# Optimization experiments

Measured on AMD Instinct MI355X. Metric: run time of the kernel, lower is better.

The kernel has to match this reference:

```python
import jax, jax.numpy as jnp
import numpy as np

D = 1024
H = 16
HD = D // H
FFN = D * 2
EPS = 1e-5


def _layernorm(x, g, b):
    mu = jnp.mean(x, axis=-1, keepdims=True)
    var = jnp.var(x, axis=-1, keepdims=True)
    return (x - mu) * jax.lax.rsqrt(var + EPS) * g + b


def setup_inputs() -> dict:
    key = jax.random.key(0)
    ks = jax.random.split(key, 12)
    s = 1.0 / np.sqrt(D)
    inp = {
        "x": jax.random.normal(ks[0], (2, 2048, D), dtype=jnp.float32),
        "Wq": jax.random.normal(ks[1], (D, D), dtype=jnp.float32) * s,
        "bq": jnp.zeros((D,), jnp.float32),
        "Wk": jax.random.normal(ks[2], (D, D), dtype=jnp.float32) * s,
        "bk": jnp.zeros((D,), jnp.float32),
        "Wv": jax.random.normal(ks[3], (D, D), dtype=jnp.float32) * s,
        "bv": jnp.zeros((D,), jnp.float32),
        "Wo": jax.random.normal(ks[4], (D, D), dtype=jnp.float32) * s,
        "bo": jnp.zeros((D,), jnp.float32),
        "g1": jnp.ones((D,), jnp.float32),
        "b1": jnp.zeros((D,), jnp.float32),
        "W_ff1": jax.random.normal(ks[5], (D, FFN), dtype=jnp.float32) * s,
        "b_ff1": jnp.zeros((FFN,), jnp.float32),
        "W_ff2": jax.random.normal(ks[6], (FFN, D), dtype=jnp.float32) * (1.0 / np.sqrt(FFN)),
        "b_ff2": jnp.zeros((D,), jnp.float32),
        "g2": jnp.ones((D,), jnp.float32),
        "b2": jnp.zeros((D,), jnp.float32),
    }
    return inp


def reference(x, Wq, bq, Wk, bk, Wv, bv, Wo, bo, g1, b1, W_ff1, b_ff1, W_ff2, b_ff2, g2, b2):
    B, S, _ = x.shape
    # QKV projections -> [B, H, S, HD]
    def split_heads(t):
        return t.reshape(B, S, H, HD).transpose(0, 2, 1, 3)
    Q = split_heads(x @ Wq + bq)
    K = split_heads(x @ Wk + bk)
    V = split_heads(x @ Wv + bv)
    scores = jnp.einsum('bhqd,bhkd->bhqk', Q, K) / np.sqrt(HD).astype(np.float32)
    attn = jax.nn.softmax(scores, axis=-1)  # dropout = identity in eval
    ctx = jnp.einsum('bhqk,bhkd->bhqd', attn, V)
    ctx = ctx.transpose(0, 2, 1, 3).reshape(B, S, D)
    x = _layernorm(x + ctx @ Wo + bo, g1, b1)
    h = jax.nn.gelu(x @ W_ff1 + b_ff1, approximate=False)
    x = _layernorm(x + h @ W_ff2 + b_ff2, g2, b2)
    return x
```

## Files before the change

kernel.cpp:

```cpp
#include <hip/hip_runtime.h>

#define SEQ 2048
#define NTOK 4096
#define DM 1024
#define LDQK 3072

typedef __attribute__((ext_vector_type(4))) float f32x4;
typedef __attribute__((ext_vector_type(8))) short short8;
typedef __attribute__((ext_vector_type(4))) short short4v;

__device__ __forceinline__ short f2bf(float f) {
  union { float f; unsigned u; } x; x.f = f;
  unsigned r = x.u + 0x7fffu + ((x.u >> 16) & 1u);
  return (short)(r >> 16);
}

__device__ __forceinline__ float bf2f(short s) {
  union { unsigned u; float f; } x;
  x.u = ((unsigned)(unsigned short)s) << 16;
  return x.f;
}

__device__ __forceinline__ void async_load16(const void* g, void* l) {
  __builtin_amdgcn_global_load_lds(
      (const __attribute__((address_space(1))) void*)g,
      (__attribute__((address_space(3))) void*)l, 16, 0, 0);
}

__global__ void __launch_bounds__(256) prep_all(
    const float* __restrict__ Wq, const float* __restrict__ Wk,
    const float* __restrict__ Wv, const float* __restrict__ Wo,
    const float* __restrict__ Wf1, const float* __restrict__ Wf2,
    const float* __restrict__ x,
    short* __restrict__ Wqkv, short* __restrict__ Wto,
    short* __restrict__ Wtf1, short* __restrict__ Wtf2,
    short* __restrict__ xb) {
  const int z = blockIdx.z;
  const int tx = threadIdx.x, ty = threadIdx.y;
  if (z == 6) {
    int blk = blockIdx.y * 64 + blockIdx.x;
    int i = blk * 256 + ty * 32 + tx;
    f32x4 v = ((const f32x4*)x)[i];
    short4v o;
#pragma unroll
    for (int j = 0; j < 4; ++j) o[j] = f2bf(v[j]);
    ((short4v*)xb)[i] = o;
    return;
  }
  const float* in;
  short* out;
  int K, N;
  switch (z) {
    case 0: in = Wq;  out = Wqkv;               K = 1024; N = 1024; break;
    case 1: in = Wk;  out = Wqkv + 1024 * 1024; K = 1024; N = 1024; break;
    case 2: in = Wv;  out = Wqkv + 2048 * 1024; K = 1024; N = 1024; break;
    case 3: in = Wo;  out = Wto;                K = 1024; N = 1024; break;
    case 4: in = Wf1; out = Wtf1;               K = 1024; N = 2048; break;
    default: in = Wf2; out = Wtf2;              K = 2048; N = 1024; break;
  }
  if (blockIdx.x * 32 >= N || blockIdx.y * 32 >= K) return;
  __shared__ float t[32][33];
  const int n = blockIdx.x * 32 + tx;
#pragma unroll
  for (int i = 0; i < 4; ++i) {
    int k = blockIdx.y * 32 + ty + i * 8;
    t[ty + i * 8][tx] = in[(size_t)k * N + n];
  }
  __syncthreads();
  const int k2 = blockIdx.y * 32 + tx;
#pragma unroll
  for (int i = 0; i < 4; ++i) {
    int n2 = blockIdx.x * 32 + ty + i * 8;
    out[(size_t)n2 * K + k2] = f2bf(t[tx][ty + i * 8]);
  }
}

template <int EPI, bool TRIPLE, bool DBUF>
__global__ void __launch_bounds__(256, 2) gemm_bt(
    const short* __restrict__ A, const short* __restrict__ Bt,
    const float* __restrict__ b0, const float* __restrict__ b1,
    const float* __restrict__ b2, void* __restrict__ Cout,
    short* __restrict__ VtOut, int M, int N, int K) {
  __shared__ __align__(16) short As[DBUF ? 2 * 128 * 64 : 128 * 64];
  __shared__ __align__(16) short Bs[DBUF ? 2 * 128 * 64 : 128 * 64];
  const int w = threadIdx.x >> 6, lane = threadIdx.x & 63;
  const int hi = lane >> 4, lo = lane & 15;
  const int bm = blockIdx.y, bn = blockIdx.x;
  const int wr = w >> 1, wc = w & 1;
  f32x4 acc[4][4] = {};
  const int nkt = K >> 6;

  auto stage = [&](int kt, int buf) {
#pragma unroll
    for (int j = 0; j < 4; ++j) {
      int c = (j * 4 + w) * 64 + lane;
      int r = c >> 3;
      int scc = (c & 7) ^ (r & 7);
      async_load16(A + (size_t)(bm * 128 + r) * K + kt * 64 + scc * 8,
                   &As[buf * (128 * 64) + (j * 4 + w) * 512]);
      async_load16(Bt + (size_t)(bn * 128 + r) * K + kt * 64 + scc * 8,
                   &Bs[buf * (128 * 64) + (j * 4 + w) * 512]);
    }
  };

  if (DBUF) {
    stage(0, 0);
    __syncthreads();
  }

  for (int kt = 0; kt < nkt; ++kt) {
    int buf = 0;
    if (DBUF) {
      buf = kt & 1;
      if (kt + 1 < nkt) stage(kt + 1, buf ^ 1);
    } else {
      stage(kt, 0);
      __syncthreads();
    }
#pragma unroll
    for (int ks = 0; ks < 2; ++ks) {
      short8 af[4], bf[4];
#pragma unroll
      for (int m = 0; m < 4; ++m) {
        int row = wr * 64 + m * 16 + lo;
        int ch = (ks * 4 + hi) ^ (row & 7);
        af[m] = *(const short8*)(&As[buf * (128 * 64) + row * 64 + ch * 8]);
      }
#pragma unroll
      for (int n = 0; n < 4; ++n) {
        int row = wc * 64 + n * 16 + lo;
        int ch = (ks * 4 + hi) ^ (row & 7);
        bf[n] = *(const short8*)(&Bs[buf * (128 * 64) + row * 64 + ch * 8]);
      }
#pragma unroll
      for (int m = 0; m < 4; ++m)
#pragma unroll
        for (int n = 0; n < 4; ++n)
          acc[m][n] = __builtin_amdgcn_mfma_f32_16x16x32_bf16(af[m], bf[n], acc[m][n], 0, 0, 0);
    }
    __syncthreads();
  }
  const float* bp = b0;
  if (TRIPLE) { int r = bn >> 3; bp = (r == 0) ? b0 : ((r == 1) ? b1 : b2); }
  const int colb = bn * 128 + wc * 64 + lo;
  if (TRIPLE && bn >= 16) {
#pragma unroll
    for (int m = 0; m < 4; ++m) {
      int row0 = bm * 128 + wr * 64 + m * 16 + hi * 4;
      int bb = row0 >> 11, ss = row0 & 2047;
#pragma unroll
      for (int n = 0; n < 4; ++n) {
        int col = colb + n * 16;
        int vdim = col - 2048;
        int hh = vdim >> 6, dd = vdim & 63;
        float bs = bp[vdim];
        short4v t;
#pragma unroll
        for (int j = 0; j < 4; ++j) t[j] = f2bf(acc[m][n][j] + bs);
        *(short4v*)&VtOut[((size_t)(bb * 16 + hh) * 64 + dd) * SEQ + ss] = t;
      }
    }
    return;
  }
#pragma unroll
  for (int m = 0; m < 4; ++m) {
    int row0 = bm * 128 + wr * 64 + m * 16 + hi * 4;
#pragma unroll
    for (int n = 0; n < 4; ++n) {
      int col = colb + n * 16;
      float bs = bp[TRIPLE ? (col & 1023) : col];
#pragma unroll
      for (int j = 0; j < 4; ++j) {
        float v = acc[m][n][j] + bs;
        if (EPI == 1) v = 0.5f * v * (1.f + erff(v * 0.70710678f));
        ((short*)Cout)[(size_t)(row0 + j) * N + col] = f2bf(v);
      }
    }
  }
}

__global__ void __launch_bounds__(256, 2) gemm_n64(
    const short* __restrict__ A, const short* __restrict__ Bt,
    const float* __restrict__ b0, const short* __restrict__ resid,
    short* __restrict__ Cout, int M, int N, int K) {
  __shared__ __align__(16) short As[2][128 * 64];
  __shared__ __align__(16) short Bs[2][64 * 64];
  const int w = threadIdx.x >> 6, lane = threadIdx.x & 63;
  const int hi = lane >> 4, lo = lane & 15;
  const int bm = blockIdx.y, bn = blockIdx.x;
  const int wr = w >> 1, wc = w & 1;
  f32x4 acc[4][2] = {};
  const int nkt = K >> 6;

  auto stage = [&](int kt, int buf) {
#pragma unroll
    for (int j = 0; j < 4; ++j) {
      int c = (j * 4 + w) * 64 + lane;
      int r = c >> 3;
      int scc = (c & 7) ^ (r & 7);
      async_load16(A + (size_t)(bm * 128 + r) * K + kt * 64 + scc * 8,
                   &As[buf][(j * 4 + w) * 512]);
    }
#pragma unroll
    for (int j = 0; j < 2; ++j) {
      int c = j * 256 + w * 64 + lane;
      int r = c >> 3;
      int scc = (c & 7) ^ (r & 7);
      async_load16(Bt + (size_t)(bn * 64 + r) * K + kt * 64 + scc * 8,
                   &Bs[buf][(j * 256 + w * 64) * 8]);
    }
  };

  stage(0, 0);
  __syncthreads();

  for (int kt = 0; kt < nkt; ++kt) {
    const int buf = kt & 1;
    if (kt + 1 < nkt) stage(kt + 1, buf ^ 1);
#pragma unroll
    for (int ks = 0; ks < 2; ++ks) {
      short8 af[4], bf[2];
#pragma unroll
      for (int m = 0; m < 4; ++m) {
        int row = wr * 64 + m * 16 + lo;
        int ch = (ks * 4 + hi) ^ (row & 7);
        af[m] = *(const short8*)(&As[buf][row * 64 + ch * 8]);
      }
#pragma unroll
      for (int n = 0; n < 2; ++n) {
        int row = wc * 32 + n * 16 + lo;
        int ch = (ks * 4 + hi) ^ (row & 7);
        bf[n] = *(const short8*)(&Bs[buf][row * 64 + ch * 8]);
      }
#pragma unroll
      for (int m = 0; m < 4; ++m)
#pragma unroll
        for (int n = 0; n < 2; ++n)
          acc[m][n] = __builtin_amdgcn_mfma_f32_16x16x32_bf16(af[m], bf[n], acc[m][n], 0, 0, 0);
    }
    __syncthreads();
  }
  const int colb = bn * 64 + wc * 32 + lo;
#pragma unroll
  for (int m = 0; m < 4; ++m) {
    int row0 = bm * 128 + wr * 64 + m * 16 + hi * 4;
#pragma unroll
    for (int n = 0; n < 2; ++n) {
      int col = colb + n * 16;
      float bs = b0[col];
#pragma unroll
      for (int j = 0; j < 4; ++j) {
        size_t idx = (size_t)(row0 + j) * N + col;
        Cout[idx] = f2bf(acc[m][n][j] + bs + bf2f(resid[idx]));
      }
    }
  }
}

__global__ void __launch_bounds__(256, 2) attn_kernel(
    const short* __restrict__ Qb, const short* __restrict__ Kb,
    const short* __restrict__ Vt, short* __restrict__ ctx) {
  const int w = threadIdx.x >> 6, lane = threadIdx.x & 63;
  const int hi = lane >> 4, lo = lane & 15;
  const int tid = threadIdx.x;
  const int L = blockIdx.y * 16 + blockIdx.x;
  const int W = (L & 7) * 64 + (L >> 3);
  const int qt = W & 15, bh = W >> 4;
  const int b = bh >> 4, h = bh & 15;
  const int qbase = qt * 128 + w * 32;
  const float C = 0.18033688f;

  __shared__ __align__(16) short Ks[2][128 * 64];
  __shared__ __align__(16) short Vs[2][64 * 128];
  __shared__ __align__(16) short P[4][16 * 128];

  const short* qp = Qb + (size_t)(b * SEQ + qbase + lo) * LDQK + h * 64;
  short8 bq[2][2];
#pragma unroll
  for (int u = 0; u < 2; ++u)
#pragma unroll
    for (int c = 0; c < 2; ++c)
      bq[u][c] = *(const short8*)(qp + (size_t)u * 16 * LDQK + c * 32 + hi * 8);

  const short* kb = Kb + (size_t)(b * SEQ) * LDQK + h * 64;
  const short* vb = Vt + (size_t)bh * 64 * SEQ;

  auto stage = [&](int kt, int buf) {
    const short* kg = kb + (size_t)(kt * 128) * LDQK;
#pragma unroll
    for (int i = 0; i < 4; ++i) {
      int c = i * 256 + tid;
      int r = c >> 3, scc = (c & 7) ^ (r & 7);
      async_load16(kg + (size_t)r * LDQK + scc * 8,
                   &Ks[buf][(i * 256 + w * 64) * 8]);
    }
    const short* vg = vb + kt * 128;
#pragma unroll
    for (int i = 0; i < 4; ++i) {
      int c = i * 256 + tid;
      int r = c >> 4, sc2 = (c & 15) ^ (r & 7);
      async_load16(vg + (size_t)r * SEQ + sc2 * 8,
                   &Vs[buf][(i * 256 + w * 64) * 8]);
    }
  };

  stage(0, 0);
  __syncthreads();

  f32x4 o[2][4] = {};
  float lacc[2] = {0.f, 0.f};
  const int x7 = lo & 7;

  for (int kt = 0; kt < SEQ / 128; ++kt) {
    const int buf = kt & 1;
    if (kt + 1 < SEQ / 128) stage(kt + 1, buf ^ 1);

    f32x4 s[2][8] = {};
#pragma unroll
    for (int g = 0; g < 8; ++g) {
      const short* kr = &Ks[buf][(g * 16 + lo) * 64];
      short8 ka0 = *(const short8*)(kr + ((hi) ^ x7) * 8);
      short8 ka1 = *(const short8*)(kr + ((4 + hi) ^ x7) * 8);
      s[0][g] = __builtin_amdgcn_mfma_f32_16x16x32_bf16(ka0, bq[0][0], s[0][g], 0, 0, 0);
      s[1][g] = __builtin_amdgcn_mfma_f32_16x16x32_bf16(ka0, bq[1][0], s[1][g], 0, 0, 0);
      s[0][g] = __builtin_amdgcn_mfma_f32_16x16x32_bf16(ka1, bq[0][1], s[0][g], 0, 0, 0);
      s[1][g] = __builtin_amdgcn_mfma_f32_16x16x32_bf16(ka1, bq[1][1], s[1][g], 0, 0, 0);
    }
    short8 vv[4][4];
#pragma unroll
    for (int ks = 0; ks < 4; ++ks)
#pragma unroll
      for (int a = 0; a < 4; ++a)
        vv[ks][a] = *(const short8*)(&Vs[buf][(a * 16 + lo) * 128 + (((ks * 4 + hi) ^ x7) * 8)]);
#pragma unroll
    for (int u = 0; u < 2; ++u) {
      float rsg[8];
      short* pbase = &P[w][0];
#pragma unroll
      for (int g = 0; g < 8; ++g) {
        float p0 = exp2f(s[u][g][0] * C);
        float p1 = exp2f(s[u][g][1] * C);
        float p2 = exp2f(s[u][g][2] * C);
        float p3 = exp2f(s[u][g][3] * C);
        rsg[g] = (p0 + p1) + (p2 + p3);
        unsigned w0, w1;
        asm("v_cvt_pk_bf16_f32 %0, %1, %2" : "=v"(w0) : "v"(p0), "v"(p1));
        asm("v_cvt_pk_bf16_f32 %0, %1, %2" : "=v"(w1) : "v"(p2), "v"(p3));
        union { unsigned uu[2]; short4v s4; } cv;
        cv.uu[0] = w0; cv.uu[1] = w1;
        int pc = (2 * g + (hi >> 1)) ^ x7;
        *(short4v*)(pbase + lo * 128 + pc * 8 + (hi & 1) * 4) = cv.s4;
      }
#pragma unroll
      for (int ks = 0; ks < 4; ++ks) {
        int pc = (ks * 4 + hi) ^ x7;
        short8 pa = *(const short8*)(pbase + lo * 128 + pc * 8);
#pragma unroll
        for (int a = 0; a < 4; ++a)
          o[u][a] = __builtin_amdgcn_mfma_f32_16x16x32_bf16(pa, vv[ks][a], o[u][a], 0, 0, 0);
      }
      lacc[u] += ((rsg[0] + rsg[1]) + (rsg[2] + rsg[3])) +
                 ((rsg[4] + rsg[5]) + (rsg[6] + rsg[7]));
    }
    __syncthreads();
  }
#pragma unroll
  for (int u = 0; u < 2; ++u) {
    lacc[u] += __shfl_xor(lacc[u], 16);
    lacc[u] += __shfl_xor(lacc[u], 32);
  }
#pragma unroll
  for (int u = 0; u < 2; ++u)
#pragma unroll
    for (int j = 0; j < 4; ++j) {
      float lj = __shfl(lacc[u], hi * 4 + j);
      float inv = 1.f / lj;
      int row = qbase + u * 16 + hi * 4 + j;
#pragma unroll
      for (int a = 0; a < 4; ++a)
        ctx[(size_t)(b * SEQ + row) * DM + h * 64 + a * 16 + lo] = f2bf(o[u][a][j] * inv);
    }
}

__global__ void __launch_bounds__(256) ln_bf16(
    const short* __restrict__ in, const float* __restrict__ g,
    const float* __restrict__ beta, float* __restrict__ outf,
    short* __restrict__ outb) {
  const int row = blockIdx.x;
  const int t = threadIdx.x;
  const size_t base = (size_t)row * DM;
  short4v iv = ((const short4v*)(in + base))[t];
  f32x4 v;
#pragma unroll
  for (int j = 0; j < 4; ++j) v[j] = bf2f(iv[j]);
  float s = v[0] + v[1] + v[2] + v[3];
  float s2 = v[0] * v[0] + v[1] * v[1] + v[2] * v[2] + v[3] * v[3];
#pragma unroll
  for (int off = 1; off < 64; off <<= 1) {
    s += __shfl_xor(s, off);
    s2 += __shfl_xor(s2, off);
  }
  __shared__ float rs[4], rs2[4];
  if ((t & 63) == 0) { rs[t >> 6] = s; rs2[t >> 6] = s2; }
  __syncthreads();
  s = rs[0] + rs[1] + rs[2] + rs[3];
  s2 = rs2[0] + rs2[1] + rs2[2] + rs2[3];
  float mu = s * (1.f / DM);
  float var = s2 * (1.f / DM) - mu * mu;
  float rstd = rsqrtf(var + 1e-5f);
  f32x4 gv = ((const f32x4*)g)[t];
  f32x4 bv = ((const f32x4*)beta)[t];
  f32x4 ov;
#pragma unroll
  for (int j = 0; j < 4; ++j) ov[j] = (v[j] - mu) * rstd * gv[j] + bv[j];
  if (outf) ((f32x4*)(outf + base))[t] = ov;
  if (outb) {
    short4v sb;
#pragma unroll
    for (int j = 0; j < 4; ++j) sb[j] = f2bf(ov[j]);
    ((short4v*)(outb + base))[t] = sb;
  }
}

extern "C" void kernel_launch(void* const* d_in, const int* in_sizes, int n_in,
                              void* d_out, int out_size, void* d_ws, size_t ws_size,
                              hipStream_t stream) {
  (void)in_sizes; (void)n_in; (void)out_size; (void)ws_size;
  const float* x   = (const float*)d_in[0];
  const float* Wq  = (const float*)d_in[1];
  const float* bq  = (const float*)d_in[2];
  const float* Wk  = (const float*)d_in[3];
  const float* bk  = (const float*)d_in[4];
  const float* Wv  = (const float*)d_in[5];
  const float* bv  = (const float*)d_in[6];
  const float* Wo  = (const float*)d_in[7];
  const float* bo  = (const float*)d_in[8];
  const float* g1  = (const float*)d_in[9];
  const float* b1  = (const float*)d_in[10];
  const float* Wf1 = (const float*)d_in[11];
  const float* bf1 = (const float*)d_in[12];
  const float* Wf2 = (const float*)d_in[13];
  const float* bf2 = (const float*)d_in[14];
  const float* g2  = (const float*)d_in[15];
  const float* b2  = (const float*)d_in[16];

  char* ws = (char*)d_ws;
  const size_t MB = 1u << 20;
  short* Wqkv = (short*)(ws + 0 * MB);
  short* Wto  = (short*)(ws + 6 * MB);
  short* Wtf1 = (short*)(ws + 8 * MB);
  short* Wtf2 = (short*)(ws + 12 * MB);
  short* xb   = (short*)(ws + 16 * MB);
  short* QKV  = (short*)(ws + 24 * MB);
  short* Vt   = (short*)(ws + 48 * MB);
  short* ctxb = (short*)(ws + 56 * MB);
  short* aout = (short*)(ws + 64 * MB);
  short* x1b  = (short*)(ws + 72 * MB);
  short* hb   = QKV;
  short* ffo  = (short*)(ws + 48 * MB);

  prep_all<<<dim3(64, 64, 7), dim3(32, 8), 0, stream>>>(
      Wq, Wk, Wv, Wo, Wf1, Wf2, x, Wqkv, Wto, Wtf1, Wtf2, xb);

  gemm_bt<0, true, false><<<dim3(24, 32), 256, 0, stream>>>(
      xb, Wqkv, bq, bk, bv, QKV, Vt, NTOK, 3072, 1024);

  attn_kernel<<<dim3(16, 32), 256, 0, stream>>>(QKV, QKV + 1024, Vt, ctxb);

  gemm_n64<<<dim3(16, 32), 256, 0, stream>>>(ctxb, Wto, bo, xb, aout, NTOK, 1024, 1024);
  ln_bf16<<<4096, 256, 0, stream>>>(aout, g1, b1, nullptr, x1b);
  gemm_bt<1, false, true><<<dim3(16, 32), 256, 0, stream>>>(
      x1b, Wtf1, bf1, bf1, bf1, hb, nullptr, NTOK, 2048, 1024);
  gemm_n64<<<dim3(16, 32), 256, 0, stream>>>(hb, Wtf2, bf2, x1b, ffo, NTOK, 1024, 2048);
  ln_bf16<<<4096, 256, 0, stream>>>(ffo, g2, b2, (float*)d_out, nullptr);
}
```

Baseline: 220.0 us.

## Shrink attention tiles to 64 queries and 64 keys per block

The attention kernel now gives each block 64 query rows (16 per wave instead of 32) and streams K/V in 64-key tiles instead of 128, which doubles the grid to 1024 blocks. Shared memory per block drops by roughly half, and so do the register arrays for scores and outputs. This is meant to raise occupancy and balance work across CUs. In exchange, each K/V tile is reused by fewer queries, so more K/V traffic and more per-tile barriers are needed.

```diff
diff --git a/kernel.cpp b/kernel.cpp
--- a/kernel.cpp
+++ b/kernel.cpp
@@ -263,42 +263,40 @@
   const int w = threadIdx.x >> 6, lane = threadIdx.x & 63;
   const int hi = lane >> 4, lo = lane & 15;
   const int tid = threadIdx.x;
-  const int L = blockIdx.y * 16 + blockIdx.x;
-  const int W = (L & 7) * 64 + (L >> 3);
-  const int qt = W & 15, bh = W >> 4;
+  const int L = blockIdx.x;
+  const int W = (L & 7) * 128 + (L >> 3);
+  const int qt = W & 31, bh = W >> 5;
   const int b = bh >> 4, h = bh & 15;
-  const int qbase = qt * 128 + w * 32;
+  const int qbase = qt * 64 + w * 16;
   const float C = 0.18033688f;
 
-  __shared__ __align__(16) short Ks[2][128 * 64];
-  __shared__ __align__(16) short Vs[2][64 * 128];
-  __shared__ __align__(16) short P[4][16 * 128];
+  __shared__ __align__(16) short Ks[2][64 * 64];
+  __shared__ __align__(16) short Vs[2][64 * 64];
+  __shared__ __align__(16) short P[4][16 * 64];
 
   const short* qp = Qb + (size_t)(b * SEQ + qbase + lo) * LDQK + h * 64;
-  short8 bq[2][2];
-#pragma unroll
-  for (int u = 0; u < 2; ++u)
-#pragma unroll
-    for (int c = 0; c < 2; ++c)
-      bq[u][c] = *(const short8*)(qp + (size_t)u * 16 * LDQK + c * 32 + hi * 8);
+  short8 bq[2];
+#pragma unroll
+  for (int c = 0; c < 2; ++c)
+    bq[c] = *(const short8*)(qp + c * 32 + hi * 8);
 
   const short* kb = Kb + (size_t)(b * SEQ) * LDQK + h * 64;
   const short* vb = Vt + (size_t)bh * 64 * SEQ;
 
   auto stage = [&](int kt, int buf) {
-    const short* kg = kb + (size_t)(kt * 128) * LDQK;
-#pragma unroll
-    for (int i = 0; i < 4; ++i) {
+    const short* kg = kb + (size_t)(kt * 64) * LDQK;
+#pragma unroll
+    for (int i = 0; i < 2; ++i) {
       int c = i * 256 + tid;
       int r = c >> 3, scc = (c & 7) ^ (r & 7);
       async_load16(kg + (size_t)r * LDQK + scc * 8,
                    &Ks[buf][(i * 256 + w * 64) * 8]);
     }
-    const short* vg = vb + kt * 128;
-#pragma unroll
-    for (int i = 0; i < 4; ++i) {
+    const short* vg = vb + kt * 64;
+#pragma unroll
+    for (int i = 0; i < 2; ++i) {
       int c = i * 256 + tid;
-      int r = c >> 4, sc2 = (c & 15) ^ (r & 7);
+      int r = c >> 3, sc2 = (c & 7) ^ (r & 7);
       async_load16(vg + (size_t)r * SEQ + sc2 * 8,
                    &Vs[buf][(i * 256 + w * 64) * 8]);
     }
@@ -307,79 +305,69 @@
   stage(0, 0);
   __syncthreads();
 
-  f32x4 o[2][4] = {};
-  float lacc[2] = {0.f, 0.f};
+  f32x4 o[4] = {};
+  float lacc = 0.f;
   const int x7 = lo & 7;
 
-  for (int kt = 0; kt < SEQ / 128; ++kt) {
+  for (int kt = 0; kt < SEQ / 64; ++kt) {
     const int buf = kt & 1;
-    if (kt + 1 < SEQ / 128) stage(kt + 1, buf ^ 1);
-
-    f32x4 s[2][8] = {};
-#pragma unroll
-    for (int g = 0; g < 8; ++g) {
+    if (kt + 1 < SEQ / 64) stage(kt + 1, buf ^ 1);
+
+    f32x4 s[4] = {};
+#pragma unroll
+    for (int g = 0; g < 4; ++g) {
       const short* kr = &Ks[buf][(g * 16 + lo) * 64];
       short8 ka0 = *(const short8*)(kr + ((hi) ^ x7) * 8);
       short8 ka1 = *(const short8*)(kr + ((4 + hi) ^ x7) * 8);
-      s[0][g] = __builtin_amdgcn_mfma_f32_16x16x32_bf16(ka0, bq[0][0], s[0][g], 0, 0, 0);
-      s[1][g] = __builtin_amdgcn_mfma_f32_16x16x32_bf16(ka0, bq[1][0], s[1][g], 0, 0, 0);
-      s[0][g] = __builtin_amdgcn_mfma_f32_16x16x32_bf16(ka1, bq[0][1], s[0][g], 0, 0, 0);
-      s[1][g] = __builtin_amdgcn_mfma_f32_16x16x32_bf16(ka1, bq[1][1], s[1][g], 0, 0, 0);
-    }
-    short8 vv[4][4];
-#pragma unroll
-    for (int ks = 0; ks < 4; ++ks)
+      s[g] = __builtin_amdgcn_mfma_f32_16x16x32_bf16(ka0, bq[0], s[g], 0, 0, 0);
+      s[g] = __builtin_amdgcn_mfma_f32_16x16x32_bf16(ka1, bq[1], s[g], 0, 0, 0);
+    }
+    short8 vv[2][4];
+#pragma unroll
+    for (int ks = 0; ks < 2; ++ks)
 #pragma unroll
       for (int a = 0; a < 4; ++a)
-        vv[ks][a] = *(const short8*)(&Vs[buf][(a * 16 + lo) * 128 + (((ks * 4 + hi) ^ x7) * 8)]);
-#pragma unroll
-    for (int u = 0; u < 2; ++u) {
-      float rsg[8];
-      short* pbase = &P[w][0];
-#pragma unroll
-      for (int g = 0; g < 8; ++g) {
-        float p0 = exp2f(s[u][g][0] * C);
-        float p1 = exp2f(s[u][g][1] * C);
-        float p2 = exp2f(s[u][g][2] * C);
-        float p3 = exp2f(s[u][g][3] * C);
-        rsg[g] = (p0 + p1) + (p2 + p3);
-        unsigned w0, w1;
-        asm("v_cvt_pk_bf16_f32 %0, %1, %2" : "=v"(w0) : "v"(p0), "v"(p1));
-        asm("v_cvt_pk_bf16_f32 %0, %1, %2" : "=v"(w1) : "v"(p2), "v"(p3));
-        union { unsigned uu[2]; short4v s4; } cv;
-        cv.uu[0] = w0; cv.uu[1] = w1;
-        int pc = (2 * g + (hi >> 1)) ^ x7;
-        *(short4v*)(pbase + lo * 128 + pc * 8 + (hi & 1) * 4) = cv.s4;
-      }
-#pragma unroll
-      for (int ks = 0; ks < 4; ++ks) {
-        int pc = (ks * 4 + hi) ^ x7;
-        short8 pa = *(const short8*)(pbase + lo * 128 + pc * 8);
-#pragma unroll
-        for (int a = 0; a < 4; ++a)
-          o[u][a] = __builtin_amdgcn_mfma_f32_16x16x32_bf16(pa, vv[ks][a], o[u][a], 0, 0, 0);
-      }
-      lacc[u] += ((rsg[0] + rsg[1]) + (rsg[2] + rsg[3])) +
-                 ((rsg[4] + rsg[5]) + (rsg[6] + rsg[7]));
-    }
+        vv[ks][a] = *(const short8*)(&Vs[buf][(a * 16 + lo) * 64 + (((ks * 4 + hi) ^ x7) * 8)]);
+
+    float rsg[4];
+    short* pbase = &P[w][0];
+#pragma unroll
+    for (int g = 0; g < 4; ++g) {
+      float p0 = exp2f(s[g][0] * C);
+      float p1 = exp2f(s[g][1] * C);
+      float p2 = exp2f(s[g][2] * C);
+      float p3 = exp2f(s[g][3] * C);
+      rsg[g] = (p0 + p1) + (p2 + p3);
+      unsigned w0, w1;
+      asm("v_cvt_pk_bf16_f32 %0, %1, %2" : "=v"(w0) : "v"(p0), "v"(p1));
+      asm("v_cvt_pk_bf16_f32 %0, %1, %2" : "=v"(w1) : "v"(p2), "v"(p3));
+      union { unsigned uu[2]; short4v s4; } cv;
+      cv.uu[0] = w0; cv.uu[1] = w1;
+      int pc = (2 * g + (hi >> 1)) ^ x7;
+      *(short4v*)(pbase + lo * 64 + pc * 8 + (hi & 1) * 4) = cv.s4;
+    }
+#pragma unroll
+    for (int ks = 0; ks < 2; ++ks) {
+      int pc = (ks * 4 + hi) ^ x7;
+      short8 pa = *(const short8*)(pbase + lo * 64 + pc * 8);
+#pragma unroll
+      for (int a = 0; a < 4; ++a)
+        o[a] = __builtin_amdgcn_mfma_f32_16x16x32_bf16(pa, vv[ks][a], o[a], 0, 0, 0);
+    }
+    lacc += (rsg[0] + rsg[1]) + (rsg[2] + rsg[3]);
     __syncthreads();
   }
-#pragma unroll
-  for (int u = 0; u < 2; ++u) {
-    lacc[u] += __shfl_xor(lacc[u], 16);
-    lacc[u] += __shfl_xor(lacc[u], 32);
-  }
-#pragma unroll
-  for (int u = 0; u < 2; ++u)
-#pragma unroll
-    for (int j = 0; j < 4; ++j) {
-      float lj = __shfl(lacc[u], hi * 4 + j);
-      float inv = 1.f / lj;
-      int row = qbase + u * 16 + hi * 4 + j;
-#pragma unroll
-      for (int a = 0; a < 4; ++a)
-        ctx[(size_t)(b * SEQ + row) * DM + h * 64 + a * 16 + lo] = f2bf(o[u][a][j] * inv);
-    }
+  lacc += __shfl_xor(lacc, 16);
+  lacc += __shfl_xor(lacc, 32);
+#pragma unroll
+  for (int j = 0; j < 4; ++j) {
+    float lj = __shfl(lacc, hi * 4 + j);
+    float inv = 1.f / lj;
+    int row = qbase + hi * 4 + j;
+#pragma unroll
+    for (int a = 0; a < 4; ++a)
+      ctx[(size_t)(b * SEQ + row) * DM + h * 64 + a * 16 + lo] = f2bf(o[a][j] * inv);
+  }
 }
 
 __global__ void __launch_bounds__(256) ln_bf16(
@@ -465,7 +453,7 @@
   gemm_bt<0, true, false><<<dim3(24, 32), 256, 0, stream>>>(
       xb, Wqkv, bq, bk, bv, QKV, Vt, NTOK, 3072, 1024);
 
-  attn_kernel<<<dim3(16, 32), 256, 0, stream>>>(QKV, QKV + 1024, Vt, ctxb);
+  attn_kernel<<<dim3(1024), 256, 0, stream>>>(QKV, QKV + 1024, Vt, ctxb);
 
   gemm_n64<<<dim3(16, 32), 256, 0, stream>>>(ctxb, Wto, bo, xb, aout, NTOK, 1024, 1024);
   ln_bf16<<<4096, 256, 0, stream>>>(aout, g1, b1, nullptr, x1b);
```

Measured after the change: 215.6 us. -2.0%, faster.
